# Optimization experiments

Measured on AMD Instinct MI355X. Metric: run time of the kernel, lower is better.

Reference implementation:

```python
import jax, jax.numpy as jnp
import numpy as np
import math

NUM_HEADS = 16  # power of two -> simple ALiBi slope formula

def alibi_slopes(num_heads: int) -> jnp.ndarray:
    # num_heads is a power of two here; general formula per Press et al. 2022
    k = 1 << (num_heads.bit_length() - 1)
    ratio = 2.0 ** (-8.0 / k)
    slopes = ratio ** np.arange(1, 1 + k)
    if num_heads != k:
        ratio2 = 2.0 ** (-8.0 / (2 * k))
        rest = (ratio2 ** np.arange(1, 1 + 2 * k, 2))[: num_heads - k]
        slopes = np.concatenate([slopes, rest])
    return jnp.asarray(slopes, dtype=jnp.float32).reshape(1, -1, 1, 1)


def setup_inputs() -> dict:
    key = jax.random.key(0)
    kq, kk, kv, km = jax.random.split(key, 4)
    B, H, S, D = 1, NUM_HEADS, 2048, 64
    query = jax.random.normal(kq, (B, H, S, D), dtype=jnp.float32)
    k_ = jax.random.normal(kk, (B, H, S, D), dtype=jnp.float32)
    value = jax.random.normal(kv, (B, H, S, D), dtype=jnp.float32)
    # padding-style boolean mask [B, S]; keep position 0 always valid
    mask = jax.random.randint(km, (B, S), 0, 2).astype(bool)
    mask = mask.at[:, 0].set(True)
    return {"query": query, "key": k_, "value": value, "mask": mask}


def reference(query, key, value, mask):
    B, H, S, D = query.shape
    scale = 1.0 / math.sqrt(D)
    # scores: [B, H, Sq, Sk]
    scores = jnp.einsum("bhqd,bhkd->bhqk", query, key) * scale
    # causal ALiBi bias: distances arange(1-S, 1) -> shape (1, H, 1, S)
    distances = jnp.arange(1 - S, 1, dtype=jnp.float32)
    bias = distances[None, None, None, :] * alibi_slopes(H)
    scores = scores + bias
    # boolean padding mask [B, S] -> [B, 1, 1, S]
    blocked = jnp.finfo(scores.dtype).min
    scores = jnp.where(mask[:, None, None, :], scores, blocked)
    weights = jax.nn.softmax(scores, axis=-1)
    # dropout_prob = 0.0 (eval) -> identity
    return jnp.einsum("bhqk,bhkd->bhqd", weights, value)
```

## Files before the change

kernel.cpp:

```cpp
#include <hip/hip_runtime.h>


constexpr int   S_LEN  = 2048;
constexpr int   D_DIM  = 64;
constexpr int   H_NUM  = 16;
constexpr int   QT     = 128;
constexpr int   K_TILE = 64;
constexpr int   NTILE  = S_LEN / K_TILE;
constexpr int   MAXNC  = 8;
constexpr int   QB     = S_LEN / QT;
constexpr int   PROWSTR= 36;
constexpr float SCL    = 0.18033688f;
constexpr float L2E    = 1.44269504f;
constexpr float MASKED = -50000.0f;
constexpr float CUTOFF = 40.0f;

typedef short bf16x8 __attribute__((ext_vector_type(8)));
typedef short bf16x4 __attribute__((ext_vector_type(4)));
typedef float f32x4  __attribute__((ext_vector_type(4)));

__device__ inline short f2bf(float f) {
    union { float f; unsigned u; } x; x.f = f;
    return (short)((x.u + 0x7fffu + ((x.u >> 16) & 1u)) >> 16);
}

__device__ inline unsigned pack2bf(float a, float b) {
#if __has_builtin(__builtin_amdgcn_cvt_pk_bf16_f32)
    auto p = __builtin_amdgcn_cvt_pk_bf16_f32(a, b);
    unsigned u; __builtin_memcpy(&u, &p, 4); return u;
#else
    return (unsigned)(unsigned short)f2bf(a) | ((unsigned)(unsigned short)f2bf(b) << 16);
#endif
}

__device__ inline float fexp2(float x) {
#if __has_builtin(__builtin_amdgcn_exp2f)
    return __builtin_amdgcn_exp2f(x);
#else
    return exp2f(x);
#endif
}

__device__ inline unsigned permb(unsigned hi, unsigned lo, unsigned sel) {
#if __has_builtin(__builtin_amdgcn_perm)
    return __builtin_amdgcn_perm(hi, lo, sel);
#else
    return (sel == 0x05040100u) ? ((lo & 0xffffu) | (hi << 16))
                                : ((lo >> 16) | (hi & 0xffff0000u));
#endif
}

__device__ inline void load_lds16(const void* g, void* l) {
    __builtin_amdgcn_global_load_lds((const __attribute__((address_space(1))) void*)g,
                                     (__attribute__((address_space(3))) void*)l, 16, 0, 0);
}

__device__ inline void store4_sc(float* p, f32x4 v) {
    asm volatile("global_store_dwordx4 %0, %1, off sc0 sc1"
                 :: "v"(p), "v"(v) : "memory");
}
__device__ inline f32x4 load4_sc(const float* p) {
    f32x4 v;
    asm volatile("global_load_dwordx4 %0, %1, off sc0 sc1"
                 : "=v"(v) : "v"(p) : "memory");
    return v;
}

__device__ inline int head_t0(int h) {
    const float slope_l2e = exp2f(-0.5f * (float)(h + 1)) * L2E;
    const float kmin = 2047.0f - CUTOFF / slope_l2e;
    return kmin <= 0.0f ? 0 : ((int)kmin) >> 6;
}
__device__ inline int head_nc(int h) {
    const int nt = NTILE - head_t0(h);
    const int nc = (nt + 3) >> 2;
    return nc > MAXNC ? MAXNC : nc;
}

__global__ __launch_bounds__(256)
void preprocess_kernel(const float* __restrict__ Km, const float* __restrict__ Vm,
                       const void* __restrict__ maskp,
                       short* __restrict__ Kswz, short* __restrict__ Vswz,
                       float* __restrict__ Bias, unsigned* __restrict__ Tickets)
{
    __shared__ int mask_is_i32;
    const int tid = threadIdx.x;
    const int kt = blockIdx.x, h = blockIdx.y;

    if (kt == 0 && tid < QB) Tickets[h * QB + tid] = 0u;

    if (kt < head_t0(h)) return;

    const int kbase = kt * K_TILE;
    const size_t tbase = ((size_t)h * S_LEN + kbase) * D_DIM;
    short* Kd = Kswz + ((size_t)h * NTILE + kt) * 4096;
    short* Vd = Vswz + ((size_t)h * NTILE + kt) * 4096;

    if (tid < 64) {
        const unsigned v = ((const unsigned*)maskp)[tid];
        const unsigned long long b = __ballot(v <= 1u);
        if (tid == 0) mask_is_i32 = (b == ~0ULL);
    }

    #pragma unroll
    for (int it = 0; it < 2; ++it) {
        const int idx = it * 256 + tid;
        const int key = idx >> 3, c = idx & 7;
        const float* src = Km + tbase + key * 64 + c * 8;
        float4 a = *(const float4*)src;
        float4 b = *(const float4*)(src + 4);
        unsigned u[4] = { pack2bf(a.x, a.y), pack2bf(a.z, a.w),
                          pack2bf(b.x, b.y), pack2bf(b.z, b.w) };
        bf16x8 kp; __builtin_memcpy(&kp, u, 16);
        *(bf16x8*)(Kd + key * 64 + ((c ^ (key & 7)) << 3)) = kp;
    }

    {
        const int db = tid >> 4, kb = tid & 15;
        const int d4 = db * 4, key4 = kb * 4;
        float4 vv[4];
        #pragma unroll
        for (int j = 0; j < 4; ++j)
            vv[j] = *(const float4*)(Vm + tbase + (key4 + j) * 64 + d4);
        const float* vp = (const float*)vv;
        #pragma unroll
        for (int jj = 0; jj < 4; ++jj) {
            const int d = d4 + jj;
            bf16x4 ov;
            ov[0] = f2bf(vp[0 * 4 + jj]); ov[1] = f2bf(vp[1 * 4 + jj]);
            ov[2] = f2bf(vp[2 * 4 + jj]); ov[3] = f2bf(vp[3 * 4 + jj]);
            *(bf16x4*)(Vd + d * 64 + (((key4 >> 3) ^ (d & 7)) << 3) + (key4 & 7)) = ov;
        }
    }
    __syncthreads();
    if (tid < K_TILE) {
        const int key = kbase + tid;
        const int mv = mask_is_i32 ? ((const int*)maskp)[key]
                                   : (int)((const unsigned char*)maskp)[key];
        const float slope_l2e = exp2f(-0.5f * (float)(h + 1)) * L2E;
        Bias[h * S_LEN + key] = mv ? slope_l2e * (float)(key - (S_LEN - 1)) : MASKED;
    }
}

__global__ __launch_bounds__(256, 4)
void attn_main(const float* __restrict__ Qm, const short* __restrict__ Kswz,
               const short* __restrict__ Vswz, const float* __restrict__ Bias,
               float* __restrict__ Om, float* __restrict__ Opart,
               float* __restrict__ lp, unsigned* __restrict__ Tickets)
{
    __shared__ short    k_lds[4096];
    __shared__ short    v_lds[4096];
    __shared__ float    bm_lds[64];
    __shared__ unsigned p_lds[4][32 * PROWSTR];
    __shared__ int      is_last;

    const int tid = threadIdx.x;
    const int wave = tid >> 6, lane = tid & 63;
    const int l16 = lane & 15, quad = lane >> 4;
    const int h = blockIdx.y, qblk = blockIdx.x, c = blockIdx.z;

    const int nc = head_nc(h);
    if (c >= nc) return;
    const int t0 = head_t0(h);
    const int nt = NTILE - t0;
    const int tstart = t0 + (c * nt) / nc;
    const int tend   = t0 + ((c + 1) * nt) / nc;

    const unsigned psel = (quad < 2) ? 0x05040100u : 0x07060302u;

    bf16x8 qfrag[2][2];
    {
        const float* Qh = Qm + (size_t)h * S_LEN * D_DIM;
        #pragma unroll
        for (int s = 0; s < 2; ++s) {
            const int qrow = qblk * QT + wave * 32 + s * 16 + l16;
            #pragma unroll
            for (int t = 0; t < 2; ++t) {
                const float* src = Qh + (size_t)qrow * D_DIM + t * 32 + quad * 8;
                float4 a = *(const float4*)src;
                float4 b = *(const float4*)(src + 4);
                unsigned* qp = (unsigned*)&qfrag[s][t];
                qp[0] = pack2bf(a.x * SCL, a.y * SCL);
                qp[1] = pack2bf(a.z * SCL, a.w * SCL);
                qp[2] = pack2bf(b.x * SCL, b.y * SCL);
                qp[3] = pack2bf(b.z * SCL, b.w * SCL);
            }
        }
    }

    bf16x8 onesv;
    #pragma unroll
    for (int i = 0; i < 8; ++i) onesv[i] = (short)0x3F80;

    f32x4 o_frag[2][4], l4[2];
    #pragma unroll
    for (int s = 0; s < 2; ++s) {
        #pragma unroll
        for (int cc = 0; cc < 4; ++cc) o_frag[s][cc] = (f32x4){0.f, 0.f, 0.f, 0.f};
        l4[s] = (f32x4){0.f, 0.f, 0.f, 0.f};
    }

    const short* Kh = Kswz + (size_t)h * NTILE * 4096;
    const short* Vh = Vswz + (size_t)h * NTILE * 4096;
    const float* Bh = Bias + h * S_LEN;
    unsigned* pw = p_lds[wave];
    const int swz = l16 & 7;

    for (int kt = tstart; kt < tend; ++kt) {
        __syncthreads();
        {
            const char* kg = (const char*)(Kh + (size_t)kt * 4096);
            const char* vg = (const char*)(Vh + (size_t)kt * 4096);
            char* kl = (char*)k_lds + wave * 2048;
            char* vl = (char*)v_lds + wave * 2048;
            const int go = wave * 2048 + lane * 16;
            load_lds16(kg + go,        kl);
            load_lds16(kg + go + 1024, kl + 1024);
            load_lds16(vg + go,        vl);
            load_lds16(vg + go + 1024, vl + 1024);
        }
        if (tid < 16) {
            float4 b4 = *(const float4*)(Bh + kt * K_TILE + tid * 4);
            *(float4*)&bm_lds[tid * 4] = b4;
        }
        __syncthreads();

        f32x4 sv[2][4];
        #pragma unroll
        for (int cc = 0; cc < 4; ++cc) {
            const float b = bm_lds[cc * 16 + l16];
            const f32x4 binit = (f32x4){b, b, b, b};
            sv[0][cc] = binit;
            sv[1][cc] = binit;
            #pragma unroll
            for (int t = 0; t < 2; ++t) {
                bf16x8 bfrag = *(const bf16x8*)&k_lds[(cc * 16 + l16) * 64 + (((t * 4 + quad) ^ swz) << 3)];
                sv[0][cc] = __builtin_amdgcn_mfma_f32_16x16x32_bf16(qfrag[0][t], bfrag, sv[0][cc], 0, 0, 0);
                sv[1][cc] = __builtin_amdgcn_mfma_f32_16x16x32_bf16(qfrag[1][t], bfrag, sv[1][cc], 0, 0, 0);
            }
        }

        #pragma unroll
        for (int s = 0; s < 2; ++s) {
            #pragma unroll
            for (int r = 0; r < 4; ++r) {
                const float p0 = fexp2(sv[s][0][r]);
                const float p1 = fexp2(sv[s][1][r]);
                const float p2 = fexp2(sv[s][2][r]);
                const float p3 = fexp2(sv[s][3][r]);
                unsigned* pp = &pw[(s * 16 + quad * 4 + r) * PROWSTR + l16];
                pp[0]  = pack2bf(p0, p1);
                pp[16] = pack2bf(p2, p3);
            }
        }

        #pragma unroll
        for (int t2 = 0; t2 < 2; ++t2) {
            bf16x8 pfrag[2];
            #pragma unroll
            for (int s = 0; s < 2; ++s) {
                const unsigned* pr = &pw[(s * 16 + l16) * PROWSTR + t2 * 16 + (quad & 1) * 8];
                uint4 w0 = *(const uint4*)(pr);
                uint4 w1 = *(const uint4*)(pr + 4);
                unsigned pf[4];
                pf[0] = permb(w0.y, w0.x, psel);
                pf[1] = permb(w0.w, w0.z, psel);
                pf[2] = permb(w1.y, w1.x, psel);
                pf[3] = permb(w1.w, w1.z, psel);
                __builtin_memcpy(&pfrag[s], pf, 16);
            }
            #pragma unroll
            for (int c2 = 0; c2 < 4; ++c2) {
                bf16x8 vfrag = *(const bf16x8*)&v_lds[(c2 * 16 + l16) * 64 + (((t2 * 4 + quad) ^ swz) << 3)];
                o_frag[0][c2] = __builtin_amdgcn_mfma_f32_16x16x32_bf16(pfrag[0], vfrag, o_frag[0][c2], 0, 0, 0);
                o_frag[1][c2] = __builtin_amdgcn_mfma_f32_16x16x32_bf16(pfrag[1], vfrag, o_frag[1][c2], 0, 0, 0);
            }
            l4[0] = __builtin_amdgcn_mfma_f32_16x16x32_bf16(pfrag[0], onesv, l4[0], 0, 0, 0);
            l4[1] = __builtin_amdgcn_mfma_f32_16x16x32_bf16(pfrag[1], onesv, l4[1], 0, 0, 0);
        }
    }

    if (nc == 1) {
        float* Oh = Om + (size_t)h * S_LEN * D_DIM;
        const int qrow0 = qblk * QT + wave * 32;
        #pragma unroll
        for (int s = 0; s < 2; ++s) {
            #pragma unroll
            for (int r = 0; r < 4; ++r) {
                const float inv = 1.0f / l4[s][r];
                const int row = qrow0 + s * 16 + quad * 4 + r;
                float* dst = Oh + (size_t)row * D_DIM + l16;
                dst[0]  = o_frag[s][0][r] * inv;
                dst[16] = o_frag[s][1][r] * inv;
                dst[32] = o_frag[s][2][r] * inv;
                dst[48] = o_frag[s][3][r] * inv;
            }
        }
    } else {
        #pragma unroll
        for (int s = 0; s < 2; ++s) {
            const int g = qblk * 32 + wave * 8 + s * 4 + quad;
            const size_t gbase = (((size_t)h * MAXNC + c) * 512 + g);
            #pragma unroll
            for (int c2 = 0; c2 < 4; ++c2)
                store4_sc(Opart + (gbase * 64 + c2 * 16 + l16) * 4, o_frag[s][c2]);
            if (l16 == 0) store4_sc(lp + gbase * 4, l4[s]);
        }

        asm volatile("s_waitcnt vmcnt(0)" ::: "memory");
        __syncthreads();
        if (tid == 0) {
            const unsigned old = atomicAdd(&Tickets[h * QB + qblk], 1u);
            is_last = (old == (unsigned)(nc - 1)) ? 1 : 0;
        }
        __syncthreads();
        if (is_last) {
            for (int cc2 = 0; cc2 < nc; ++cc2) {
                if (cc2 == c) continue;
                f32x4 t[2][4], tl[2];
                #pragma unroll
                for (int s = 0; s < 2; ++s) {
                    const int g = qblk * 32 + wave * 8 + s * 4 + quad;
                    const size_t gbase = (((size_t)h * MAXNC + cc2) * 512 + g);
                    tl[s] = load4_sc(lp + gbase * 4);
                    #pragma unroll
                    for (int c2 = 0; c2 < 4; ++c2)
                        t[s][c2] = load4_sc(Opart + (gbase * 64 + c2 * 16 + l16) * 4);
                }
                asm volatile("s_waitcnt vmcnt(0)" ::: "memory");
                __builtin_amdgcn_sched_barrier(0);
                #pragma unroll
                for (int s = 0; s < 2; ++s) {
                    l4[s] += tl[s];
                    #pragma unroll
                    for (int c2 = 0; c2 < 4; ++c2) o_frag[s][c2] += t[s][c2];
                }
            }
            float* Oh = Om + (size_t)h * S_LEN * D_DIM;
            const int qrow0 = qblk * QT + wave * 32;
            #pragma unroll
            for (int s = 0; s < 2; ++s) {
                #pragma unroll
                for (int r = 0; r < 4; ++r) {
                    const float inv = 1.0f / l4[s][r];
                    const int row = qrow0 + s * 16 + quad * 4 + r;
                    float* dst = Oh + (size_t)row * D_DIM + l16;
                    dst[0]  = o_frag[s][0][r] * inv;
                    dst[16] = o_frag[s][1][r] * inv;
                    dst[32] = o_frag[s][2][r] * inv;
                    dst[48] = o_frag[s][3][r] * inv;
                }
            }
        }
    }
}

extern "C" void kernel_launch(void* const* d_in, const int* in_sizes, int n_in,
                              void* d_out, int out_size, void* d_ws, size_t ws_size,
                              hipStream_t stream) {
    (void)in_sizes; (void)n_in; (void)out_size; (void)ws_size;
    const float* Q = (const float*)d_in[0];
    const float* K = (const float*)d_in[1];
    const float* V = (const float*)d_in[2];
    const void*  M = d_in[3];
    float* O = (float*)d_out;

    char* ws = (char*)d_ws;
    size_t off = 0;
    short* Kswz = (short*)(ws + off); off += (size_t)H_NUM * S_LEN * D_DIM * 2;
    short* Vswz = (short*)(ws + off); off += (size_t)H_NUM * S_LEN * D_DIM * 2;
    float* Bias = (float*)(ws + off); off += (size_t)H_NUM * S_LEN * 4;
    float* Opart = (float*)(ws + off); off += (size_t)H_NUM * MAXNC * 512 * 64 * 4 * 4;
    float* lp   = (float*)(ws + off); off += (size_t)H_NUM * MAXNC * 512 * 4 * 4;
    unsigned* Tickets = (unsigned*)(ws + off); off += (size_t)H_NUM * QB * 4;

    preprocess_kernel<<<dim3(NTILE, H_NUM), 256, 0, stream>>>(K, V, M, Kswz, Vswz, Bias, Tickets);
    attn_main<<<dim3(QB, H_NUM, MAXNC), 256, 0, stream>>>(Q, Kswz, Vswz, Bias, O, Opart, lp, Tickets);
}
```

Before: 99.01 us.

## Prefetch next K/V tile into registers and preload ALiBi bias for the chunk

Global loads for the next K/V tile are now issued into registers at the top of each iteration and written into LDS after the current tile's MFMAs, so load latency overlaps compute. The bias values for all tiles in the block's chunk are loaded into LDS once before the loop. Wave priority is raised around the MFMA sections. The LDS stays single-buffered, so two barriers per iteration remain, the prefetched registers raise register pressure, and the enlarged bias buffer only holds four tiles, which is correct only if no chunk spans more than four tiles.

```diff
diff --git a/kernel.cpp b/kernel.cpp
--- a/kernel.cpp
+++ b/kernel.cpp
@@ -150,7 +150,7 @@
 {
     __shared__ short    k_lds[4096];
     __shared__ short    v_lds[4096];
-    __shared__ float    bm_lds[64];
+    __shared__ float    bm_lds[256];
     __shared__ unsigned p_lds[4][32 * PROWSTR];
     __shared__ int      is_last;
 
@@ -167,6 +167,28 @@
     const int tend   = t0 + ((c + 1) * nt) / nc;
 
     const unsigned psel = (quad < 2) ? 0x05040100u : 0x07060302u;
+    const short* Kh = Kswz + (size_t)h * NTILE * 4096;
+    const short* Vh = Vswz + (size_t)h * NTILE * 4096;
+    const float* Bh = Bias + h * S_LEN;
+    unsigned* pw = p_lds[wave];
+    const int swz = l16 & 7;
+    const int go  = wave * 2048 + lane * 16;
+
+    {
+        const int tt = tid >> 6;
+        if (tt < tend - tstart)
+            bm_lds[tid] = Bh[(tstart + tt) * K_TILE + (tid & 63)];
+    }
+    {
+        const char* kg = (const char*)(Kh + (size_t)tstart * 4096);
+        const char* vg = (const char*)(Vh + (size_t)tstart * 4096);
+        char* kl = (char*)k_lds + wave * 2048;
+        char* vl = (char*)v_lds + wave * 2048;
+        load_lds16(kg + go,        kl);
+        load_lds16(kg + go + 1024, kl + 1024);
+        load_lds16(vg + go,        vl);
+        load_lds16(vg + go + 1024, vl + 1024);
+    }
 
     bf16x8 qfrag[2][2];
     {
@@ -200,35 +222,28 @@
         l4[s] = (f32x4){0.f, 0.f, 0.f, 0.f};
     }
 
-    const short* Kh = Kswz + (size_t)h * NTILE * 4096;
-    const short* Vh = Vswz + (size_t)h * NTILE * 4096;
-    const float* Bh = Bias + h * S_LEN;
-    unsigned* pw = p_lds[wave];
-    const int swz = l16 & 7;
+    __syncthreads();
 
     for (int kt = tstart; kt < tend; ++kt) {
-        __syncthreads();
-        {
-            const char* kg = (const char*)(Kh + (size_t)kt * 4096);
-            const char* vg = (const char*)(Vh + (size_t)kt * 4096);
-            char* kl = (char*)k_lds + wave * 2048;
-            char* vl = (char*)v_lds + wave * 2048;
-            const int go = wave * 2048 + lane * 16;
-            load_lds16(kg + go,        kl);
-            load_lds16(kg + go + 1024, kl + 1024);
-            load_lds16(vg + go,        vl);
-            load_lds16(vg + go + 1024, vl + 1024);
-        }
-        if (tid < 16) {
-            float4 b4 = *(const float4*)(Bh + kt * K_TILE + tid * 4);
-            *(float4*)&bm_lds[tid * 4] = b4;
-        }
-        __syncthreads();
+        const bool pre = (kt + 1 < tend);
+        uint4 kr0, kr1, vr0, vr1;
+        if (pre) {
+            const char* kg2 = (const char*)(Kh + (size_t)(kt + 1) * 4096);
+            const char* vg2 = (const char*)(Vh + (size_t)(kt + 1) * 4096);
+            kr0 = *(const uint4*)(kg2 + go);
+            kr1 = *(const uint4*)(kg2 + go + 1024);
+            vr0 = *(const uint4*)(vg2 + go);
+            vr1 = *(const uint4*)(vg2 + go + 1024);
+        }
+        __builtin_amdgcn_sched_barrier(0);
+
+        const float* bm = &bm_lds[(kt - tstart) * K_TILE];
 
         f32x4 sv[2][4];
+        __builtin_amdgcn_s_setprio(1);
         #pragma unroll
         for (int cc = 0; cc < 4; ++cc) {
-            const float b = bm_lds[cc * 16 + l16];
+            const float b = bm[cc * 16 + l16];
             const f32x4 binit = (f32x4){b, b, b, b};
             sv[0][cc] = binit;
             sv[1][cc] = binit;
@@ -239,6 +254,7 @@
                 sv[1][cc] = __builtin_amdgcn_mfma_f32_16x16x32_bf16(qfrag[1][t], bfrag, sv[1][cc], 0, 0, 0);
             }
         }
+        __builtin_amdgcn_s_setprio(0);
 
         #pragma unroll
         for (int s = 0; s < 2; ++s) {
@@ -269,6 +285,7 @@
                 pf[3] = permb(w1.w, w1.z, psel);
                 __builtin_memcpy(&pfrag[s], pf, 16);
             }
+            __builtin_amdgcn_s_setprio(1);
             #pragma unroll
             for (int c2 = 0; c2 < 4; ++c2) {
                 bf16x8 vfrag = *(const bf16x8*)&v_lds[(c2 * 16 + l16) * 64 + (((t2 * 4 + quad) ^ swz) << 3)];
@@ -277,6 +294,18 @@
             }
             l4[0] = __builtin_amdgcn_mfma_f32_16x16x32_bf16(pfrag[0], onesv, l4[0], 0, 0, 0);
             l4[1] = __builtin_amdgcn_mfma_f32_16x16x32_bf16(pfrag[1], onesv, l4[1], 0, 0, 0);
+            __builtin_amdgcn_s_setprio(0);
+        }
+
+        if (pre) {
+            __syncthreads();
+            char* kl = (char*)k_lds + go;
+            char* vl = (char*)v_lds + go;
+            *(uint4*)kl          = kr0;
+            *(uint4*)(kl + 1024) = kr1;
+            *(uint4*)vl          = vr0;
+            *(uint4*)(vl + 1024) = vr1;
+            __syncthreads();
         }
     }
 
```

Measured after the change: 100.5 us. Within noise of the previous version (+1.5%).

## Fuse K/V bf16 conversion and bias into attention kernel with register prefetch

Applied to the files above, without the earlier changes.

Removes the separate preprocess kernel. The attention kernel now loads fp32 K/V tiles straight from global memory into registers, converts them to swizzled bf16 in LDS, and computes ALiBi/mask bias per chunk into LDS. The next tile is prefetched into registers while the current one is computed, and MFMA sections get s_setprio hints. Ticket reset moves to hipMemsetAsync. This cuts a launch and the workspace round trip, but each query block now redoes the fp32 conversion for its key range, which adds redundant global reads and VALU work, and it uses more registers.

```diff
diff --git a/kernel.cpp b/kernel.cpp
--- a/kernel.cpp
+++ b/kernel.cpp
@@ -50,11 +50,6 @@
 #endif
 }
 
-__device__ inline void load_lds16(const void* g, void* l) {
-    __builtin_amdgcn_global_load_lds((const __attribute__((address_space(1))) void*)g,
-                                     (__attribute__((address_space(3))) void*)l, 16, 0, 0);
-}
-
 __device__ inline void store4_sc(float* p, f32x4 v) {
     asm volatile("global_store_dwordx4 %0, %1, off sc0 sc1"
                  :: "v"(p), "v"(v) : "memory");
@@ -77,82 +72,18 @@
     return nc > MAXNC ? MAXNC : nc;
 }
 
-__global__ __launch_bounds__(256)
-void preprocess_kernel(const float* __restrict__ Km, const float* __restrict__ Vm,
-                       const void* __restrict__ maskp,
-                       short* __restrict__ Kswz, short* __restrict__ Vswz,
-                       float* __restrict__ Bias, unsigned* __restrict__ Tickets)
-{
-    __shared__ int mask_is_i32;
-    const int tid = threadIdx.x;
-    const int kt = blockIdx.x, h = blockIdx.y;
-
-    if (kt == 0 && tid < QB) Tickets[h * QB + tid] = 0u;
-
-    if (kt < head_t0(h)) return;
-
-    const int kbase = kt * K_TILE;
-    const size_t tbase = ((size_t)h * S_LEN + kbase) * D_DIM;
-    short* Kd = Kswz + ((size_t)h * NTILE + kt) * 4096;
-    short* Vd = Vswz + ((size_t)h * NTILE + kt) * 4096;
-
-    if (tid < 64) {
-        const unsigned v = ((const unsigned*)maskp)[tid];
-        const unsigned long long b = __ballot(v <= 1u);
-        if (tid == 0) mask_is_i32 = (b == ~0ULL);
-    }
-
-    #pragma unroll
-    for (int it = 0; it < 2; ++it) {
-        const int idx = it * 256 + tid;
-        const int key = idx >> 3, c = idx & 7;
-        const float* src = Km + tbase + key * 64 + c * 8;
-        float4 a = *(const float4*)src;
-        float4 b = *(const float4*)(src + 4);
-        unsigned u[4] = { pack2bf(a.x, a.y), pack2bf(a.z, a.w),
-                          pack2bf(b.x, b.y), pack2bf(b.z, b.w) };
-        bf16x8 kp; __builtin_memcpy(&kp, u, 16);
-        *(bf16x8*)(Kd + key * 64 + ((c ^ (key & 7)) << 3)) = kp;
-    }
-
-    {
-        const int db = tid >> 4, kb = tid & 15;
-        const int d4 = db * 4, key4 = kb * 4;
-        float4 vv[4];
-        #pragma unroll
-        for (int j = 0; j < 4; ++j)
-            vv[j] = *(const float4*)(Vm + tbase + (key4 + j) * 64 + d4);
-        const float* vp = (const float*)vv;
-        #pragma unroll
-        for (int jj = 0; jj < 4; ++jj) {
-            const int d = d4 + jj;
-            bf16x4 ov;
-            ov[0] = f2bf(vp[0 * 4 + jj]); ov[1] = f2bf(vp[1 * 4 + jj]);
-            ov[2] = f2bf(vp[2 * 4 + jj]); ov[3] = f2bf(vp[3 * 4 + jj]);
-            *(bf16x4*)(Vd + d * 64 + (((key4 >> 3) ^ (d & 7)) << 3) + (key4 & 7)) = ov;
-        }
-    }
-    __syncthreads();
-    if (tid < K_TILE) {
-        const int key = kbase + tid;
-        const int mv = mask_is_i32 ? ((const int*)maskp)[key]
-                                   : (int)((const unsigned char*)maskp)[key];
-        const float slope_l2e = exp2f(-0.5f * (float)(h + 1)) * L2E;
-        Bias[h * S_LEN + key] = mv ? slope_l2e * (float)(key - (S_LEN - 1)) : MASKED;
-    }
-}
-
 __global__ __launch_bounds__(256, 4)
-void attn_main(const float* __restrict__ Qm, const short* __restrict__ Kswz,
-               const short* __restrict__ Vswz, const float* __restrict__ Bias,
-               float* __restrict__ Om, float* __restrict__ Opart,
-               float* __restrict__ lp, unsigned* __restrict__ Tickets)
+void attn_all(const float* __restrict__ Qm, const float* __restrict__ Km,
+              const float* __restrict__ Vm, const void* __restrict__ maskp,
+              float* __restrict__ Om, float* __restrict__ Opart,
+              float* __restrict__ lp, unsigned* __restrict__ Tickets)
 {
     __shared__ short    k_lds[4096];
     __shared__ short    v_lds[4096];
-    __shared__ float    bm_lds[64];
+    __shared__ float    bias_lds[256];
     __shared__ unsigned p_lds[4][32 * PROWSTR];
     __shared__ int      is_last;
+    __shared__ int      mask_is_i32;
 
     const int tid = threadIdx.x;
     const int wave = tid >> 6, lane = tid & 63;
@@ -166,11 +97,64 @@
     const int tstart = t0 + (c * nt) / nc;
     const int tend   = t0 + ((c + 1) * nt) / nc;
 
-    const unsigned psel = (quad < 2) ? 0x05040100u : 0x07060302u;
+    const int key0 = tid >> 3, c0 = tid & 7;
+    const int db = tid >> 4, kb = tid & 15;
+    const int d4 = db * 4, key4 = kb * 4;
+
+    const size_t hbase = (size_t)h * S_LEN * D_DIM;
+
+    if (tid < 64) {
+        const unsigned v = ((const unsigned*)maskp)[tid];
+        const unsigned long long b = __ballot(v <= 1u);
+        if (tid == 0) mask_is_i32 = (b == ~0ULL);
+    }
+
+    float4 kr0, kr1, kr2, kr3, vr0, vr1, vr2, vr3;
+
+    #define STAGE_LOAD(KT)                                                     \
+    do {                                                                       \
+        const float* tbK = Km + hbase + (size_t)(KT) * K_TILE * D_DIM;         \
+        const float* s0 = tbK + key0 * 64 + c0 * 8;                            \
+        kr0 = *(const float4*)s0;  kr1 = *(const float4*)(s0 + 4);             \
+        const float* s1 = tbK + (key0 + 32) * 64 + c0 * 8;                     \
+        kr2 = *(const float4*)s1;  kr3 = *(const float4*)(s1 + 4);             \
+        const float* tbV = Vm + hbase + (size_t)(KT) * K_TILE * D_DIM;         \
+        vr0 = *(const float4*)(tbV + (key4 + 0) * 64 + d4);                    \
+        vr1 = *(const float4*)(tbV + (key4 + 1) * 64 + d4);                    \
+        vr2 = *(const float4*)(tbV + (key4 + 2) * 64 + d4);                    \
+        vr3 = *(const float4*)(tbV + (key4 + 3) * 64 + d4);                    \
+    } while (0)
+
+    #define STAGE_WRITE()                                                      \
+    do {                                                                       \
+        unsigned ua[4] = { pack2bf(kr0.x, kr0.y), pack2bf(kr0.z, kr0.w),       \
+                           pack2bf(kr1.x, kr1.y), pack2bf(kr1.z, kr1.w) };     \
+        bf16x8 kpa; __builtin_memcpy(&kpa, ua, 16);                            \
+        *(bf16x8*)&k_lds[key0 * 64 + ((c0 ^ (key0 & 7)) << 3)] = kpa;          \
+        unsigned ub[4] = { pack2bf(kr2.x, kr2.y), pack2bf(kr2.z, kr2.w),       \
+                           pack2bf(kr3.x, kr3.y), pack2bf(kr3.z, kr3.w) };     \
+        bf16x8 kpb; __builtin_memcpy(&kpb, ub, 16);                            \
+        const int key1 = key0 + 32;                                           \
+        *(bf16x8*)&k_lds[key1 * 64 + ((c0 ^ (key1 & 7)) << 3)] = kpb;          \
+        const float* vp0 = (const float*)&vr0;                                 \
+        const float* vp1 = (const float*)&vr1;                                 \
+        const float* vp2 = (const float*)&vr2;                                 \
+        const float* vp3 = (const float*)&vr3;                                 \
+        _Pragma("unroll")                                                      \
+        for (int jj = 0; jj < 4; ++jj) {                                       \
+            const int d = d4 + jj;                                             \
+            bf16x4 ov;                                                         \
+            ov[0] = f2bf(vp0[jj]); ov[1] = f2bf(vp1[jj]);                      \
+            ov[2] = f2bf(vp2[jj]); ov[3] = f2bf(vp3[jj]);                      \
+            *(bf16x4*)&v_lds[d * 64 + (((key4 >> 3) ^ (d & 7)) << 3) + (key4 & 7)] = ov; \
+        }                                                                      \
+    } while (0)
+
+    STAGE_LOAD(tstart);
 
     bf16x8 qfrag[2][2];
     {
-        const float* Qh = Qm + (size_t)h * S_LEN * D_DIM;
+        const float* Qh = Qm + hbase;
         #pragma unroll
         for (int s = 0; s < 2; ++s) {
             const int qrow = qblk * QT + wave * 32 + s * 16 + l16;
@@ -200,35 +184,38 @@
         l4[s] = (f32x4){0.f, 0.f, 0.f, 0.f};
     }
 
-    const short* Kh = Kswz + (size_t)h * NTILE * 4096;
-    const short* Vh = Vswz + (size_t)h * NTILE * 4096;
-    const float* Bh = Bias + h * S_LEN;
+    __syncthreads();
+
+    {
+        const int tt = tid >> 6, kk = tid & 63;
+        if (tstart + tt < tend) {
+            const int key = (tstart + tt) * K_TILE + kk;
+            const int mv = mask_is_i32 ? ((const int*)maskp)[key]
+                                       : (int)((const unsigned char*)maskp)[key];
+            const float slope_l2e = exp2f(-0.5f * (float)(h + 1)) * L2E;
+            bias_lds[tid] = mv ? slope_l2e * (float)(key - (S_LEN - 1)) : MASKED;
+        }
+    }
+
+    STAGE_WRITE();
+    __syncthreads();
+
+    const unsigned psel = (quad < 2) ? 0x05040100u : 0x07060302u;
     unsigned* pw = p_lds[wave];
     const int swz = l16 & 7;
 
     for (int kt = tstart; kt < tend; ++kt) {
-        __syncthreads();
-        {
-            const char* kg = (const char*)(Kh + (size_t)kt * 4096);
-            const char* vg = (const char*)(Vh + (size_t)kt * 4096);
-            char* kl = (char*)k_lds + wave * 2048;
-            char* vl = (char*)v_lds + wave * 2048;
-            const int go = wave * 2048 + lane * 16;
-            load_lds16(kg + go,        kl);
-            load_lds16(kg + go + 1024, kl + 1024);
-            load_lds16(vg + go,        vl);
-            load_lds16(vg + go + 1024, vl + 1024);
-        }
-        if (tid < 16) {
-            float4 b4 = *(const float4*)(Bh + kt * K_TILE + tid * 4);
-            *(float4*)&bm_lds[tid * 4] = b4;
-        }
-        __syncthreads();
+        const bool pre = (kt + 1 < tend);
+        if (pre) STAGE_LOAD(kt + 1);
+        __builtin_amdgcn_sched_barrier(0);
+
+        const float* bm = &bias_lds[(kt - tstart) * K_TILE];
 
         f32x4 sv[2][4];
+        __builtin_amdgcn_s_setprio(1);
         #pragma unroll
         for (int cc = 0; cc < 4; ++cc) {
-            const float b = bm_lds[cc * 16 + l16];
+            const float b = bm[cc * 16 + l16];
             const f32x4 binit = (f32x4){b, b, b, b};
             sv[0][cc] = binit;
             sv[1][cc] = binit;
@@ -239,6 +226,7 @@
                 sv[1][cc] = __builtin_amdgcn_mfma_f32_16x16x32_bf16(qfrag[1][t], bfrag, sv[1][cc], 0, 0, 0);
             }
         }
+        __builtin_amdgcn_s_setprio(0);
 
         #pragma unroll
         for (int s = 0; s < 2; ++s) {
@@ -269,6 +257,7 @@
                 pf[3] = permb(w1.w, w1.z, psel);
                 __builtin_memcpy(&pfrag[s], pf, 16);
             }
+            __builtin_amdgcn_s_setprio(1);
             #pragma unroll
             for (int c2 = 0; c2 < 4; ++c2) {
                 bf16x8 vfrag = *(const bf16x8*)&v_lds[(c2 * 16 + l16) * 64 + (((t2 * 4 + quad) ^ swz) << 3)];
@@ -277,11 +266,18 @@
             }
             l4[0] = __builtin_amdgcn_mfma_f32_16x16x32_bf16(pfrag[0], onesv, l4[0], 0, 0, 0);
             l4[1] = __builtin_amdgcn_mfma_f32_16x16x32_bf16(pfrag[1], onesv, l4[1], 0, 0, 0);
+            __builtin_amdgcn_s_setprio(0);
+        }
+
+        if (pre) {
+            __syncthreads();
+            STAGE_WRITE();
+            __syncthreads();
         }
     }
 
     if (nc == 1) {
-        float* Oh = Om + (size_t)h * S_LEN * D_DIM;
+        float* Oh = Om + hbase;
         const int qrow0 = qblk * QT + wave * 32;
         #pragma unroll
         for (int s = 0; s < 2; ++s) {
@@ -336,7 +332,7 @@
                     for (int c2 = 0; c2 < 4; ++c2) o_frag[s][c2] += t[s][c2];
                 }
             }
-            float* Oh = Om + (size_t)h * S_LEN * D_DIM;
+            float* Oh = Om + hbase;
             const int qrow0 = qblk * QT + wave * 32;
             #pragma unroll
             for (int s = 0; s < 2; ++s) {
@@ -353,6 +349,8 @@
             }
         }
     }
+    #undef STAGE_LOAD
+    #undef STAGE_WRITE
 }
 
 extern "C" void kernel_launch(void* const* d_in, const int* in_sizes, int n_in,
@@ -367,13 +365,10 @@
 
     char* ws = (char*)d_ws;
     size_t off = 0;
-    short* Kswz = (short*)(ws + off); off += (size_t)H_NUM * S_LEN * D_DIM * 2;
-    short* Vswz = (short*)(ws + off); off += (size_t)H_NUM * S_LEN * D_DIM * 2;
-    float* Bias = (float*)(ws + off); off += (size_t)H_NUM * S_LEN * 4;
     float* Opart = (float*)(ws + off); off += (size_t)H_NUM * MAXNC * 512 * 64 * 4 * 4;
-    float* lp   = (float*)(ws + off); off += (size_t)H_NUM * MAXNC * 512 * 4 * 4;
+    float* lp    = (float*)(ws + off); off += (size_t)H_NUM * MAXNC * 512 * 4 * 4;
     unsigned* Tickets = (unsigned*)(ws + off); off += (size_t)H_NUM * QB * 4;
 
-    preprocess_kernel<<<dim3(NTILE, H_NUM), 256, 0, stream>>>(K, V, M, Kswz, Vswz, Bias, Tickets);
-    attn_main<<<dim3(QB, H_NUM, MAXNC), 256, 0, stream>>>(Q, Kswz, Vswz, Bias, O, Opart, lp, Tickets);
-}
+    hipMemsetAsync(Tickets, 0, (size_t)H_NUM * QB * 4, stream);
+    attn_all<<<dim3(QB, H_NUM, MAXNC), 256, 0, stream>>>(Q, K, V, M, O, Opart, lp, Tickets);
+}
```

Result: slower. 171.9 us (+73.6%).
